# Kernel optimization log

Measured on AMD Instinct MI355X. Metric: run time of the kernel, lower is better.

Reference implementation:

```python
import jax, jax.numpy as jnp
import numpy as np

K = 20
EPS = 1e-5
NEG_SLOPE = 0.2


def knn(x, k):
    # x: [B, C, N] -> idx [B, N, k] of nearest neighbors (negative sq-dist topk)
    inner = -2.0 * jnp.einsum('bcn,bcm->bnm', x, x)
    xx = jnp.sum(x * x, axis=1)  # [B, N]
    d = -xx[:, :, None] - inner - xx[:, None, :]
    return jax.lax.top_k(d, k)[1]


def get_graph_feature(x, k):
    # x: [B, C, N] -> [B, 2C, N, k]
    idx = knn(x, k)
    xt = jnp.transpose(x, (0, 2, 1))            # [B, N, C]
    feat = jax.vmap(lambda a, i: a[i])(xt, idx)  # [B, N, k, C]
    center = xt[:, :, None, :]
    out = jnp.concatenate([feat - center, jnp.broadcast_to(center, feat.shape)], axis=-1)
    return jnp.transpose(out, (0, 3, 1, 2))


def conv_bn_lrelu(x, w, g, b):
    # 1x1 conv + BatchNorm2d (batch stats, training mode) + LeakyReLU(0.2)
    y = jnp.einsum('oc,bcnk->bonk', w, x)
    mu = jnp.mean(y, axis=(0, 2, 3), keepdims=True)
    var = jnp.mean((y - mu) ** 2, axis=(0, 2, 3), keepdims=True)
    y = (y - mu) * jax.lax.rsqrt(var + EPS)
    y = y * g[None, :, None, None] + b[None, :, None, None]
    return jnp.where(y >= 0, y, NEG_SLOPE * y)


def lrelu(y):
    return jnp.where(y >= 0, y, NEG_SLOPE * y)


def setup_inputs() -> dict:
    key = jax.random.key(0)
    ks = jax.random.split(key, 24)
    B, N = 8, 4096
    d = {}
    d['x'] = jax.random.normal(ks[0], (B, 3, N), dtype=jnp.float32)
    def wconv(k_, o, c):
        return jax.random.normal(k_, (o, c), dtype=jnp.float32) * (1.0 / np.sqrt(c))
    d['w1'] = wconv(ks[1], 32, 6)
    d['g1'] = 1.0 + 0.1 * jax.random.normal(ks[2], (32,), dtype=jnp.float32)
    d['b1'] = 0.1 * jax.random.normal(ks[3], (32,), dtype=jnp.float32)
    d['w2'] = wconv(ks[4], 64, 70)
    d['g2'] = 1.0 + 0.1 * jax.random.normal(ks[5], (64,), dtype=jnp.float32)
    d['b2'] = 0.1 * jax.random.normal(ks[6], (64,), dtype=jnp.float32)
    d['wd1'] = wconv(ks[7], 64, 64)
    d['gd1'] = 1.0 + 0.1 * jax.random.normal(ks[8], (64,), dtype=jnp.float32)
    d['bd1'] = 0.1 * jax.random.normal(ks[9], (64,), dtype=jnp.float32)
    d['wd2'] = wconv(ks[10], 64, 128)
    d['gd2'] = 1.0 + 0.1 * jax.random.normal(ks[11], (64,), dtype=jnp.float32)
    d['bd2'] = 0.1 * jax.random.normal(ks[12], (64,), dtype=jnp.float32)
    d['W2d'] = jax.random.normal(ks[13], (128, 128), dtype=jnp.float32) * (1.0 / np.sqrt(128))
    d['b2d'] = 0.1 * jax.random.normal(ks[14], (128,), dtype=jnp.float32)
    d['W3d'] = jax.random.normal(ks[15], (64, 128), dtype=jnp.float32) * (1.0 / np.sqrt(128))
    d['b3d'] = 0.1 * jax.random.normal(ks[16], (64,), dtype=jnp.float32)
    d['W4d'] = jax.random.normal(ks[17], (11, 64), dtype=jnp.float32) * (1.0 / np.sqrt(64))
    d['b4d'] = 0.1 * jax.random.normal(ks[18], (11,), dtype=jnp.float32)
    return d


def reference(x, w1, g1, b1, w2, g2, b2, wd1, gd1, bd1, wd2, gd2, bd2,
              W2d, b2d, W3d, b3d, W4d, b4d):
    x1_gf = get_graph_feature(x, K)                    # [B, 6, N, k]
    x1_max = jnp.max(conv_bn_lrelu(x1_gf, w1, g1, b1), axis=-1)  # [B, 32, N]
    x2_gf = jnp.concatenate([x1_gf, get_graph_feature(x1_max, K)], axis=1)  # [B, 70, N, k]
    x2_max = jnp.max(conv_bn_lrelu(x2_gf, w2, g2, b2), axis=-1)  # [B, 64, N]
    xd1 = jnp.max(conv_bn_lrelu(get_graph_feature(x1_max, K), wd1, gd1, bd1), axis=-1)  # [B, 64, N]
    xd2 = jnp.max(conv_bn_lrelu(get_graph_feature(x2_max, K), wd2, gd2, bd2), axis=-1)  # [B, 64, N]
    h = jnp.concatenate([xd1, xd2], axis=1)            # [B, 128, N]
    h = h.reshape(1, -1, 128)                          # faithful row-major view
    h = jnp.mean(h, axis=1)                            # [1, 128]
    h = lrelu(h @ W2d.T + b2d)
    h = lrelu(h @ W3d.T + b3d)
    return lrelu(h @ W4d.T + b4d)                      # [1, 11]
```

## Files before the change

kernel.cpp:

```cpp
#include <hip/hip_runtime.h>

#define BB 8
#define NN 4096
#define KK 20
constexpr float EPSV = 1e-5f;
constexpr float SLOPE = 0.2f;

typedef __bf16 bfrag __attribute__((ext_vector_type(8)));
typedef float floatx4 __attribute__((ext_vector_type(4)));
typedef unsigned short us4 __attribute__((ext_vector_type(4)));
typedef unsigned short us8 __attribute__((ext_vector_type(8)));

__device__ __forceinline__ float lrelu(float v) { return v >= 0.f ? v : SLOPE * v; }

__device__ __forceinline__ unsigned short bf16rn(float f) {
    unsigned int u = __float_as_uint(f);
    return (unsigned short)((u + 0x7FFFu + ((u >> 16) & 1u)) >> 16);
}
__device__ __forceinline__ float bf16up(unsigned short h) {
    return __uint_as_float(((unsigned int)h) << 16);
}

__device__ __forceinline__ void gl_lds16(const unsigned short* g, unsigned short* l) {
    __builtin_amdgcn_global_load_lds((const __attribute__((address_space(1))) void*)g,
                                     (__attribute__((address_space(3))) void*)l, 16, 0, 0);
}

__global__ void zero_kernel(float* p, int n) {
    int i = blockIdx.x * 256 + threadIdx.x;
    if (i < n) p[i] = 0.f;
}

template<int C>
__global__ void halfnorm_kernel(const float* __restrict__ src, float* __restrict__ hng) {
    int n = blockIdx.x * 256 + threadIdx.x;
    int b = blockIdx.y;
    float s = 0.f;
    #pragma unroll
    for (int c = 0; c < C; c++) { float v = src[(b * C + c) * NN + n]; s += v * v; }
    hng[b * NN + n] = 0.5f * s;
}

template<int C>
__global__ void pack_kernel(const float* __restrict__ src, const float* __restrict__ hng,
                            unsigned short* __restrict__ pk) {
    constexpr int SK = 2 * C + 8;
    const int b = blockIdx.y;
    const int m0 = blockIdx.x * 64;
    const int tid = threadIdx.x;
    for (int i = tid; i < 64 * (C / 4); i += 256) {
        int m = i & 63;
        int c4 = (i >> 6) * 4;
        us4 hv, lv;
        #pragma unroll
        for (int j = 0; j < 4; j++) {
            float v = src[(b * C + c4 + j) * NN + m0 + m];
            unsigned short h = bf16rn(v);
            hv[j] = h;
            lv[j] = bf16rn(v - bf16up(h));
        }
        *(us4*)(&pk[(size_t)(b * NN + m0 + m) * SK + c4]) = hv;
        *(us4*)(&pk[(size_t)(b * NN + m0 + m) * SK + C + c4]) = lv;
    }
    if (tid < 64) {
        unsigned int ub = __float_as_uint(hng[b * NN + m0 + tid]);
        us8 z;
        #pragma unroll
        for (int j = 0; j < 8; j++) z[j] = 0;
        z[0] = (unsigned short)(ub & 0xFFFFu);
        z[1] = (unsigned short)(ub >> 16);
        *(us8*)(&pk[(size_t)(b * NN + m0 + tid) * SK + 2 * C]) = z;
    }
}

__global__ void pack3_kernel(const float* __restrict__ src, const float* __restrict__ hng,
                             unsigned short* __restrict__ pk) {
    const int b = blockIdx.y;
    const int m = blockIdx.x * 256 + threadIdx.x;
    us8 w0, w1;
    #pragma unroll
    for (int j = 0; j < 8; j++) { w0[j] = 0; w1[j] = 0; }
    unsigned short row[12];
    #pragma unroll
    for (int c = 0; c < 3; c++) {
        float v = src[(b * 3 + c) * NN + m];
        unsigned short h = bf16rn(v);
        unsigned short l = bf16rn(v - bf16up(h));
        row[c] = h; row[3 + c] = l; row[6 + c] = l; row[9 + c] = h;
    }
    #pragma unroll
    for (int j = 0; j < 8; j++) w0[j] = row[j];
    #pragma unroll
    for (int j = 0; j < 4; j++) w1[j] = row[8 + j];
    unsigned short* dst = pk + (size_t)(b * NN + m) * 40;
    us8 z;
    #pragma unroll
    for (int j = 0; j < 8; j++) z[j] = 0;
    unsigned int ub = __float_as_uint(hng[b * NN + m]);
    us8 zh = z;
    zh[0] = (unsigned short)(ub & 0xFFFFu);
    zh[1] = (unsigned short)(ub >> 16);
    *(us8*)(dst) = w0;
    *(us8*)(dst + 8) = w1;
    *(us8*)(dst + 16) = z;
    *(us8*)(dst + 24) = z;
    *(us8*)(dst + 32) = zh;
}

template<int C>
__global__ __launch_bounds__(256) void knn_kernel(const float* __restrict__ src,
                                                  const unsigned short* __restrict__ pk,
                                                  int* __restrict__ idx) {
    constexpr int SK = (C == 3) ? 40 : (2 * C + 8);
    constexpr int HNOFF = (C == 3) ? 32 : 2 * C;
    constexpr int UNITS = 8 * SK;
    constexpr int PF = (UNITS + 255) / 256;
    constexpr int KKN = (C == 3) ? 1 : (C / 32);
    __shared__ __attribute__((aligned(16))) unsigned short cpack[2 * 64 * SK];
    __shared__ float pv[64 * 65];
    __shared__ unsigned short pidx[64 * 66];
    __shared__ float tau[64];
    __shared__ int cnt[64];
    __shared__ unsigned short qls[(C == 3) ? 64 * 40 : 2];

    const int bid = blockIdx.x;
    const int b = bid & 7;
    const int q0 = (bid >> 3) * 64;
    const int tid = threadIdx.x;
    const int lane = tid & 63;
    const int wv = tid >> 6;
    const int wr = (wv >> 1) * 32;
    const int wc = (wv & 1) * 32;
    const int fl = lane & 15;
    const int fq = lane >> 4;

    float tv[20]; int ti[20];
    #pragma unroll
    for (int k = 0; k < 20; k++) { tv[k] = -3.4e38f; ti[k] = 0; }

    bfrag qah[KKN][2], qal[KKN][2];
    if (C == 3) {
        for (int i = tid; i < 64 * 20; i += 256) {
            int r = i / 20, k = 12 + i % 20;
            qls[r * 40 + k] = 0;
        }
        if (tid < 64) {
            #pragma unroll
            for (int c = 0; c < 3; c++) {
                float v = src[(b * 3 + c) * NN + q0 + tid];
                unsigned short h = bf16rn(v);
                unsigned short l = bf16rn(v - bf16up(h));
                qls[tid * 40 + c] = h;  qls[tid * 40 + 3 + c] = l;
                qls[tid * 40 + 6 + c] = h;  qls[tid * 40 + 9 + c] = l;
            }
        }
    } else {
        #pragma unroll
        for (int r2 = 0; r2 < 2; r2++) {
            const unsigned short* qr = pk + (size_t)(b * NN + q0 + wr + r2 * 16 + fl) * SK + fq * 8;
            #pragma unroll
            for (int kk = 0; kk < KKN; kk++) {
                qah[kk][r2] = *(const bfrag*)(qr + kk * 32);
                qal[kk][r2] = *(const bfrag*)(qr + C + kk * 32);
            }
        }
    }

    {
        const unsigned short* p0 = pk + (size_t)(b * NN) * SK;
        #pragma unroll
        for (int r = 0; r < PF; r++) {
            int u0 = r * 256 + wv * 64;
            if (u0 < UNITS)
                gl_lds16(p0 + (size_t)(u0 + lane) * 8, cpack + (size_t)u0 * 8);
        }
    }
    if (tid < 64) { tau[tid] = -3.4e38f; cnt[tid] = 0; }
    __syncthreads();

    bfrag qa3[2];
    if (C == 3) {
        #pragma unroll
        for (int r2 = 0; r2 < 2; r2++)
            qa3[r2] = *(const bfrag*)(&qls[(wr + r2 * 16 + fl) * 40 + fq * 8]);
    }

    int buf = 0;
    for (int ch = 0; ch < 64; ch++) {
        unsigned short* cur = cpack + buf * (64 * SK);
        if (ch + 1 < 64) {
            unsigned short* nxt = cpack + (buf ^ 1) * (64 * SK);
            const unsigned short* pn = pk + (size_t)(b * NN + (ch + 1) * 64) * SK;
            #pragma unroll
            for (int r = 0; r < PF; r++) {
                int u0 = r * 256 + wv * 64;
                if (u0 < UNITS)
                    gl_lds16(pn + (size_t)(u0 + lane) * 8, nxt + (size_t)u0 * 8);
            }
        }

        floatx4 acc[2][2];
        #pragma unroll
        for (int r2 = 0; r2 < 2; r2++)
            #pragma unroll
            for (int c2 = 0; c2 < 2; c2++)
                acc[r2][c2] = (floatx4)(0.f);

        if (C == 3) {
            #pragma unroll
            for (int c2 = 0; c2 < 2; c2++) {
                bfrag bm = *(const bfrag*)(&cur[(wc + c2 * 16 + fl) * SK + fq * 8]);
                #pragma unroll
                for (int r2 = 0; r2 < 2; r2++)
                    acc[r2][c2] = __builtin_amdgcn_mfma_f32_16x16x32_bf16(qa3[r2], bm, acc[r2][c2], 0, 0, 0);
            }
        } else {
            #pragma unroll
            for (int kk = 0; kk < KKN; kk++) {
                const int kb = kk * 32 + fq * 8;
                bfrag bh[2], bl[2];
                #pragma unroll
                for (int c2 = 0; c2 < 2; c2++) {
                    bh[c2] = *(const bfrag*)(&cur[(wc + c2 * 16 + fl) * SK + kb]);
                    bl[c2] = *(const bfrag*)(&cur[(wc + c2 * 16 + fl) * SK + C + kb]);
                }
                #pragma unroll
                for (int r2 = 0; r2 < 2; r2++)
                    #pragma unroll
                    for (int c2 = 0; c2 < 2; c2++) {
                        acc[r2][c2] = __builtin_amdgcn_mfma_f32_16x16x32_bf16(qah[kk][r2], bh[c2], acc[r2][c2], 0, 0, 0);
                        acc[r2][c2] = __builtin_amdgcn_mfma_f32_16x16x32_bf16(qah[kk][r2], bl[c2], acc[r2][c2], 0, 0, 0);
                        acc[r2][c2] = __builtin_amdgcn_mfma_f32_16x16x32_bf16(qal[kk][r2], bh[c2], acc[r2][c2], 0, 0, 0);
                        acc[r2][c2] = __builtin_amdgcn_mfma_f32_16x16x32_bf16(qal[kk][r2], bl[c2], acc[r2][c2], 0, 0, 0);
                    }
            }
        }

        {
            const int m0 = ch * 64;
            float hvv[2];
            #pragma unroll
            for (int c2 = 0; c2 < 2; c2++)
                hvv[c2] = *(const float*)(&cur[(wc + c2 * 16 + fl) * SK + HNOFF]);
            #pragma unroll
            for (int r2 = 0; r2 < 2; r2++) {
                const int qb = wr + r2 * 16 + fq * 4;
                float4 t4 = *(const float4*)(&tau[qb]);
                float ta[4] = { t4.x, t4.y, t4.z, t4.w };
                #pragma unroll
                for (int c2 = 0; c2 < 2; c2++) {
                    const float hv = hvv[c2];
                    const int mm = m0 + wc + c2 * 16 + fl;
                    #pragma unroll
                    for (int reg = 0; reg < 4; reg++) {
                        float s = acc[r2][c2][reg] - hv;
                        if (s > ta[reg]) {
                            int q = qb + reg;
                            int p = atomicAdd(&cnt[q], 1);
                            pv[q * 65 + p] = s;
                            pidx[q * 66 + p] = (unsigned short)mm;
                        }
                    }
                }
            }
        }
        __syncthreads();

        if (tid < 64) {
            int n = cnt[tid];
            for (int t = 0; t < n; t++) {
                float v = pv[tid * 65 + t];
                if (v > tv[0]) {
                    tv[0] = v; ti[0] = (int)pidx[tid * 66 + t];
                    #pragma unroll
                    for (int j = 0; j < 19; j++) {
                        if (tv[j] > tv[j + 1]) {
                            float a = tv[j]; tv[j] = tv[j + 1]; tv[j + 1] = a;
                            int bi = ti[j]; ti[j] = ti[j + 1]; ti[j + 1] = bi;
                        }
                    }
                }
            }
            cnt[tid] = 0;
            tau[tid] = tv[0];
        }
        __syncthreads();
        buf ^= 1;
    }

    if (tid < 64) {
        #pragma unroll
        for (int k = 0; k < 20; k++)
            idx[(b * NN + q0 + tid) * KK + k] = ti[k];
    }
}

template<int COUT>
__global__ void precompute_kernel(const float* __restrict__ src, int C,
                                  const float* __restrict__ w, int CIN, int wd_off, int wc_off,
                                  float* __restrict__ G, float* __restrict__ H,
                                  int initG, int initH) {
    constexpr int MY = 256 / COUT;
    extern __shared__ float lds[];
    float* wd = lds;
    float* wc = lds + C * COUT;
    const int b = blockIdx.y;
    const int tid = threadIdx.y * COUT + threadIdx.x;
    for (int i = tid; i < C * COUT; i += 256) {
        int c = i / COUT, o = i % COUT;
        float a  = w[o * CIN + wd_off + c];
        float cc = w[o * CIN + wc_off + c];
        wd[i] = a;
        wc[i] = cc - a;
    }
    __syncthreads();
    const int o = threadIdx.x;
    for (int it = 0; it < COUT / 4; it++) {
        int m = blockIdx.x * 64 + it * MY + threadIdx.y;
        float g = 0.f, h = 0.f;
        for (int c = 0; c < C; c++) {
            float s = src[(b * C + c) * NN + m];
            g += wd[c * COUT + o] * s;
            h += wc[c * COUT + o] * s;
        }
        int gi = (b * NN + m) * COUT + o;
        if (initG) G[gi] = g; else G[gi] += g;
        if (initH) H[gi] = h; else H[gi] += h;
    }
}

template<int COUT, int GROUPS>
__global__ void conv_stats_kernel(const float* __restrict__ G1, const int* __restrict__ idx1,
                                  const float* __restrict__ G2, const int* __restrict__ idx2,
                                  const float* __restrict__ H, float* __restrict__ stats,
                                  float* __restrict__ MaxY, float* __restrict__ MinY) {
    constexpr int NY = 256 / COUT;
    const int b = blockIdx.y;
    const int o = threadIdx.x;
    const int n = blockIdx.x * NY + threadIdx.y;
    const int base = b * NN + n;
    const float h = H[base * COUT + o];
    float s1 = 0.f, s2 = 0.f;
    float gx = -3.4e38f, gn = 3.4e38f;
    #pragma unroll
    for (int k = 0; k < KK; k++) {
        int i1 = idx1[base * KK + k];
        float g = G1[(b * NN + i1) * COUT + o];
        if (GROUPS == 2) {
            int i2 = idx2[base * KK + k];
            g += G2[(b * NN + i2) * COUT + o];
        }
        float y = g + h;
        s1 += y;
        s2 += y * y;
        gx = fmaxf(gx, g);
        gn = fminf(gn, g);
    }
    MaxY[base * COUT + o] = gx + h;
    MinY[base * COUT + o] = gn + h;

    __shared__ float ls[2 * COUT];
    if (threadIdx.y == 0) { ls[o] = 0.f; ls[COUT + o] = 0.f; }
    __syncthreads();
    atomicAdd(&ls[o], s1);
    atomicAdd(&ls[COUT + o], s2);
    __syncthreads();
    if (threadIdx.y == 0) {
        atomicAdd(&stats[o], ls[o]);
        atomicAdd(&stats[64 + o], ls[COUT + o]);
    }
}

__global__ void finalize_kernel(const float* __restrict__ g, const float* __restrict__ bb,
                                float* __restrict__ stats, int cout, float invP) {
    int o = threadIdx.x;
    if (o >= cout) return;
    float mu  = stats[o] * invP;
    float var = stats[64 + o] * invP - mu * mu;
    float sc  = g[o] * rsqrtf(var + EPSV);
    stats[128 + o] = sc;
    stats[192 + o] = bb[o] - mu * sc;
}

__global__ void apply_kernel(const float* __restrict__ MaxY, const float* __restrict__ MinY,
                             const float* __restrict__ stats, float* __restrict__ out, int cout) {
    int e = blockIdx.x * 256 + threadIdx.x;
    int total = BB * cout * NN;
    if (e >= total) return;
    int n = e & (NN - 1);
    int o = (e >> 12) % cout;
    int b = e / (NN * cout);
    float sc = stats[128 + o], sh = stats[192 + o];
    int si = (b * NN + n) * cout + o;
    float v = (sc >= 0.f) ? MaxY[si] : MinY[si];
    out[e] = lrelu(sc * v + sh);
}

__global__ void mean_kernel(const float* __restrict__ xd1, const float* __restrict__ xd2,
                            float* __restrict__ hsum) {
    __shared__ float bins[128];
    const int tid = threadIdx.x;
    if (tid < 128) bins[tid] = 0.f;
    __syncthreads();
    const int half = BB * 64 * NN;
    const int stride = gridDim.x * 256;
    for (int e = blockIdx.x * 256 + tid; e < half; e += stride)
        atomicAdd(&bins[e & 127], xd1[e]);
    for (int e = blockIdx.x * 256 + tid; e < half; e += stride)
        atomicAdd(&bins[e & 127], xd2[e]);
    __syncthreads();
    if (tid < 128) atomicAdd(&hsum[tid], bins[tid]);
}

__global__ void head_kernel(const float* __restrict__ hsum,
                            const float* __restrict__ W2d, const float* __restrict__ b2d,
                            const float* __restrict__ W3d, const float* __restrict__ b3d,
                            const float* __restrict__ W4d, const float* __restrict__ b4d,
                            float* __restrict__ out) {
    __shared__ float h[128], t1[128], t2[64];
    const int t = threadIdx.x;
    h[t] = hsum[t] * (1.f / 32768.f);
    __syncthreads();
    float a = b2d[t];
    for (int j = 0; j < 128; j++) a += W2d[t * 128 + j] * h[j];
    t1[t] = lrelu(a);
    __syncthreads();
    if (t < 64) {
        float a2 = b3d[t];
        for (int j = 0; j < 128; j++) a2 += W3d[t * 128 + j] * t1[j];
        t2[t] = lrelu(a2);
    }
    __syncthreads();
    if (t < 11) {
        float a3 = b4d[t];
        for (int j = 0; j < 64; j++) a3 += W4d[t * 64 + j] * t2[j];
        out[t] = lrelu(a3);
    }
}

extern "C" void kernel_launch(void* const* d_in, const int* in_sizes, int n_in,
                              void* d_out, int out_size, void* d_ws, size_t ws_size,
                              hipStream_t stream) {
    const float* x   = (const float*)d_in[0];
    const float* w1  = (const float*)d_in[1];
    const float* g1  = (const float*)d_in[2];
    const float* b1  = (const float*)d_in[3];
    const float* w2  = (const float*)d_in[4];
    const float* g2  = (const float*)d_in[5];
    const float* b2  = (const float*)d_in[6];
    const float* wd1 = (const float*)d_in[7];
    const float* gd1 = (const float*)d_in[8];
    const float* bd1 = (const float*)d_in[9];
    const float* wd2 = (const float*)d_in[10];
    const float* gd2 = (const float*)d_in[11];
    const float* bd2 = (const float*)d_in[12];
    const float* W2d = (const float*)d_in[13];
    const float* b2d = (const float*)d_in[14];
    const float* W3d = (const float*)d_in[15];
    const float* b3d = (const float*)d_in[16];
    const float* W4d = (const float*)d_in[17];
    const float* b4d = (const float*)d_in[18];
    float* out = (float*)d_out;

    char* ws = (char*)d_ws;
    size_t off = 0;
    auto alloc = [&](size_t bytes) { char* p = ws + off; off += (bytes + 255) & ~size_t(255); return p; };
    int*   idx1  = (int*)  alloc(BB * NN * KK * 4);
    int*   idx2  = (int*)  alloc(BB * NN * KK * 4);
    int*   idx3  = (int*)  alloc(BB * NN * KK * 4);
    float* x1m   = (float*)alloc(BB * 32 * NN * 4);
    float* x2m   = (float*)alloc(BB * 64 * NN * 4);
    float* xd1   = (float*)alloc(BB * 64 * NN * 4);
    float* xd2   = (float*)alloc(BB * 64 * NN * 4);
    float* G1    = (float*)alloc((size_t)BB * NN * 64 * 4);
    float* G2    = (float*)alloc((size_t)BB * NN * 64 * 4);
    float* H     = (float*)alloc((size_t)BB * NN * 64 * 4);
    float* MaxY  = (float*)alloc((size_t)BB * NN * 64 * 4);
    float* MinY  = (float*)alloc((size_t)BB * NN * 64 * 4);
    float* stats = (float*)alloc(256 * 4);
    float* hsum  = (float*)alloc(128 * 4);
    float* hng   = (float*)alloc(BB * NN * 4);

    unsigned short* pkbuf = (unsigned short*)MaxY;

    const float invP = 1.f / (float)(BB * NN * KK);
    const dim3 knn_grid(NN / 64 * BB);
    const dim3 hn_grid(NN / 256, BB);

    zero_kernel<<<1, 256, 0, stream>>>(hsum, 128);

    halfnorm_kernel<3><<<hn_grid, 256, 0, stream>>>(x, hng);
    pack3_kernel<<<dim3(NN / 256, BB), 256, 0, stream>>>(x, hng, pkbuf);
    knn_kernel<3><<<knn_grid, 256, 0, stream>>>(x, pkbuf, idx1);

    zero_kernel<<<1, 256, 0, stream>>>(stats, 128);
    precompute_kernel<32><<<dim3(NN / 64, BB), dim3(32, 8), 2 * 3 * 32 * 4, stream>>>(
        x, 3, w1, 6, 0, 3, G1, H, 1, 1);
    conv_stats_kernel<32, 1><<<dim3(NN / 8, BB), dim3(32, 8), 0, stream>>>(
        G1, idx1, nullptr, nullptr, H, stats, MaxY, MinY);
    finalize_kernel<<<1, 64, 0, stream>>>(g1, b1, stats, 32, invP);
    apply_kernel<<<(BB * 32 * NN + 255) / 256, 256, 0, stream>>>(MaxY, MinY, stats, x1m, 32);

    halfnorm_kernel<32><<<hn_grid, 256, 0, stream>>>(x1m, hng);
    pack_kernel<32><<<dim3(NN / 64, BB), 256, 0, stream>>>(x1m, hng, pkbuf);
    knn_kernel<32><<<knn_grid, 256, 0, stream>>>(x1m, pkbuf, idx2);

    zero_kernel<<<1, 256, 0, stream>>>(stats, 128);
    precompute_kernel<64><<<dim3(NN / 64, BB), dim3(64, 4), 2 * 3 * 64 * 4, stream>>>(
        x, 3, w2, 70, 0, 3, G1, H, 1, 1);
    precompute_kernel<64><<<dim3(NN / 64, BB), dim3(64, 4), 2 * 32 * 64 * 4, stream>>>(
        x1m, 32, w2, 70, 6, 38, G2, H, 1, 0);
    conv_stats_kernel<64, 2><<<dim3(NN / 4, BB), dim3(64, 4), 0, stream>>>(
        G1, idx1, G2, idx2, H, stats, MaxY, MinY);
    finalize_kernel<<<1, 64, 0, stream>>>(g2, b2, stats, 64, invP);
    apply_kernel<<<(BB * 64 * NN + 255) / 256, 256, 0, stream>>>(MaxY, MinY, stats, x2m, 64);

    zero_kernel<<<1, 256, 0, stream>>>(stats, 128);
    precompute_kernel<64><<<dim3(NN / 64, BB), dim3(64, 4), 2 * 32 * 64 * 4, stream>>>(
        x1m, 32, wd1, 64, 0, 32, G1, H, 1, 1);
    conv_stats_kernel<64, 1><<<dim3(NN / 4, BB), dim3(64, 4), 0, stream>>>(
        G1, idx2, nullptr, nullptr, H, stats, MaxY, MinY);
    finalize_kernel<<<1, 64, 0, stream>>>(gd1, bd1, stats, 64, invP);
    apply_kernel<<<(BB * 64 * NN + 255) / 256, 256, 0, stream>>>(MaxY, MinY, stats, xd1, 64);

    halfnorm_kernel<64><<<hn_grid, 256, 0, stream>>>(x2m, hng);
    pack_kernel<64><<<dim3(NN / 64, BB), 256, 0, stream>>>(x2m, hng, pkbuf);
    knn_kernel<64><<<knn_grid, 256, 0, stream>>>(x2m, pkbuf, idx3);

    zero_kernel<<<1, 256, 0, stream>>>(stats, 128);
    precompute_kernel<64><<<dim3(NN / 64, BB), dim3(64, 4), 2 * 64 * 64 * 4, stream>>>(
        x2m, 64, wd2, 128, 0, 64, G1, H, 1, 1);
    conv_stats_kernel<64, 1><<<dim3(NN / 4, BB), dim3(64, 4), 0, stream>>>(
        G1, idx3, nullptr, nullptr, H, stats, MaxY, MinY);
    finalize_kernel<<<1, 64, 0, stream>>>(gd2, bd2, stats, 64, invP);
    apply_kernel<<<(BB * 64 * NN + 255) / 256, 256, 0, stream>>>(MaxY, MinY, stats, xd2, 64);

    mean_kernel<<<1024, 256, 0, stream>>>(xd1, xd2, hsum);
    head_kernel<<<1, 128, 0, stream>>>(hsum, W2d, b2d, W3d, b3d, W4d, b4d, out);
}
```

Before: 1.706 ms.

## Double KNN block query tile and overlap top-k merge with next MFMA chunk

The KNN kernel now handles 128 queries per block with 512 threads, so each candidate chunk loaded into LDS is reused across twice as many queries. The per-chunk top-k insertion pass, which ran between two barriers, now runs at the start of the next iteration and reads candidates from a 128-entry ring buffer using a running lo/hi count. This removes one barrier per chunk and lets the serial merge by 128 threads overlap with MFMA work in the other waves. The trade-offs are that tau is one chunk staler, which admits more candidates, the ring can overflow if more than 128 candidates build up per query before a merge, and the grid has half as many blocks.

```diff
diff --git a/kernel.cpp b/kernel.cpp
--- a/kernel.cpp
+++ b/kernel.cpp
@@ -108,24 +108,25 @@
 }
 
 template<int C>
-__global__ __launch_bounds__(256) void knn_kernel(const float* __restrict__ src,
+__global__ __launch_bounds__(512) void knn_kernel(const float* __restrict__ src,
                                                   const unsigned short* __restrict__ pk,
                                                   int* __restrict__ idx) {
     constexpr int SK = (C == 3) ? 40 : (2 * C + 8);
     constexpr int HNOFF = (C == 3) ? 32 : 2 * C;
     constexpr int UNITS = 8 * SK;
-    constexpr int PF = (UNITS + 255) / 256;
+    constexpr int CHUNK = 64 * SK;
+    constexpr int RU = (UNITS + 511) / 512;
     constexpr int KKN = (C == 3) ? 1 : (C / 32);
-    __shared__ __attribute__((aligned(16))) unsigned short cpack[2 * 64 * SK];
-    __shared__ float pv[64 * 65];
-    __shared__ unsigned short pidx[64 * 66];
-    __shared__ float tau[64];
-    __shared__ int cnt[64];
-    __shared__ unsigned short qls[(C == 3) ? 64 * 40 : 2];
+    constexpr int PVS = 130, PIS = 129;
+    __shared__ __attribute__((aligned(16))) unsigned short cpack[2 * CHUNK];
+    __shared__ __attribute__((aligned(16))) float pv[128 * PVS];
+    __shared__ unsigned short pidx[128 * PIS];
+    __shared__ float tau[128];
+    __shared__ int cnt[128];
 
     const int bid = blockIdx.x;
     const int b = bid & 7;
-    const int q0 = (bid >> 3) * 64;
+    const int q0 = (bid >> 3) * 128;
     const int tid = threadIdx.x;
     const int lane = tid & 63;
     const int wv = tid >> 6;
@@ -140,11 +141,10 @@
 
     bfrag qah[KKN][2], qal[KKN][2];
     if (C == 3) {
-        for (int i = tid; i < 64 * 20; i += 256) {
-            int r = i / 20, k = 12 + i % 20;
-            qls[r * 40 + k] = 0;
-        }
-        if (tid < 64) {
+        unsigned short* qls = (unsigned short*)pv;
+        if (tid < 128) {
+            #pragma unroll
+            for (int k2 = 12; k2 < 32; k2++) qls[tid * 40 + k2] = 0;
             #pragma unroll
             for (int c = 0; c < 3; c++) {
                 float v = src[(b * 3 + c) * NN + q0 + tid];
@@ -169,34 +169,56 @@
     {
         const unsigned short* p0 = pk + (size_t)(b * NN) * SK;
         #pragma unroll
-        for (int r = 0; r < PF; r++) {
-            int u0 = r * 256 + wv * 64;
+        for (int r = 0; r < RU; r++) {
+            int u0 = r * 512 + wv * 64;
             if (u0 < UNITS)
                 gl_lds16(p0 + (size_t)(u0 + lane) * 8, cpack + (size_t)u0 * 8);
         }
     }
-    if (tid < 64) { tau[tid] = -3.4e38f; cnt[tid] = 0; }
+    if (tid < 128) { tau[tid] = -3.4e38f; cnt[tid] = 0; }
     __syncthreads();
 
     bfrag qa3[2];
     if (C == 3) {
+        const unsigned short* qls = (const unsigned short*)pv;
         #pragma unroll
         for (int r2 = 0; r2 < 2; r2++)
             qa3[r2] = *(const bfrag*)(&qls[(wr + r2 * 16 + fl) * 40 + fq * 8]);
-    }
-
-    int buf = 0;
+        __syncthreads();
+    }
+
+    int lo = 0;
     for (int ch = 0; ch < 64; ch++) {
-        unsigned short* cur = cpack + buf * (64 * SK);
+        const unsigned short* cur = cpack + (ch & 1) * CHUNK;
         if (ch + 1 < 64) {
-            unsigned short* nxt = cpack + (buf ^ 1) * (64 * SK);
+            unsigned short* nxt = cpack + ((ch + 1) & 1) * CHUNK;
             const unsigned short* pn = pk + (size_t)(b * NN + (ch + 1) * 64) * SK;
             #pragma unroll
-            for (int r = 0; r < PF; r++) {
-                int u0 = r * 256 + wv * 64;
+            for (int r = 0; r < RU; r++) {
+                int u0 = r * 512 + wv * 64;
                 if (u0 < UNITS)
                     gl_lds16(pn + (size_t)(u0 + lane) * 8, nxt + (size_t)u0 * 8);
             }
+        }
+
+        if (tid < 128) {
+            int hi = cnt[tid];
+            for (int t = lo; t < hi; t++) {
+                int s = t & 127;
+                float v = pv[tid * PVS + s];
+                if (v > tv[0]) {
+                    tv[0] = v; ti[0] = (int)pidx[tid * PIS + s];
+                    #pragma unroll
+                    for (int j = 0; j < 19; j++) {
+                        if (tv[j] > tv[j + 1]) {
+                            float a = tv[j]; tv[j] = tv[j + 1]; tv[j + 1] = a;
+                            int bi = ti[j]; ti[j] = ti[j + 1]; ti[j + 1] = bi;
+                        }
+                    }
+                }
+            }
+            lo = hi;
+            tau[tid] = tv[0];
         }
 
         floatx4 acc[2][2];
@@ -257,38 +279,33 @@
                         if (s > ta[reg]) {
                             int q = qb + reg;
                             int p = atomicAdd(&cnt[q], 1);
-                            pv[q * 65 + p] = s;
-                            pidx[q * 66 + p] = (unsigned short)mm;
+                            int sl = p & 127;
+                            pv[q * PVS + sl] = s;
+                            pidx[q * PIS + sl] = (unsigned short)mm;
                         }
                     }
                 }
             }
         }
         __syncthreads();
-
-        if (tid < 64) {
-            int n = cnt[tid];
-            for (int t = 0; t < n; t++) {
-                float v = pv[tid * 65 + t];
-                if (v > tv[0]) {
-                    tv[0] = v; ti[0] = (int)pidx[tid * 66 + t];
-                    #pragma unroll
-                    for (int j = 0; j < 19; j++) {
-                        if (tv[j] > tv[j + 1]) {
-                            float a = tv[j]; tv[j] = tv[j + 1]; tv[j + 1] = a;
-                            int bi = ti[j]; ti[j] = ti[j + 1]; ti[j + 1] = bi;
-                        }
+    }
+
+    if (tid < 128) {
+        int hi = cnt[tid];
+        for (int t = lo; t < hi; t++) {
+            int s = t & 127;
+            float v = pv[tid * PVS + s];
+            if (v > tv[0]) {
+                tv[0] = v; ti[0] = (int)pidx[tid * PIS + s];
+                #pragma unroll
+                for (int j = 0; j < 19; j++) {
+                    if (tv[j] > tv[j + 1]) {
+                        float a = tv[j]; tv[j] = tv[j + 1]; tv[j + 1] = a;
+                        int bi = ti[j]; ti[j] = ti[j + 1]; ti[j + 1] = bi;
                     }
                 }
             }
-            cnt[tid] = 0;
-            tau[tid] = tv[0];
-        }
-        __syncthreads();
-        buf ^= 1;
-    }
-
-    if (tid < 64) {
+        }
         #pragma unroll
         for (int k = 0; k < 20; k++)
             idx[(b * NN + q0 + tid) * KK + k] = ti[k];
@@ -484,14 +501,14 @@
     unsigned short* pkbuf = (unsigned short*)MaxY;
 
     const float invP = 1.f / (float)(BB * NN * KK);
-    const dim3 knn_grid(NN / 64 * BB);
+    const dim3 knn_grid(NN / 128 * BB);
     const dim3 hn_grid(NN / 256, BB);
 
     zero_kernel<<<1, 256, 0, stream>>>(hsum, 128);
 
     halfnorm_kernel<3><<<hn_grid, 256, 0, stream>>>(x, hng);
     pack3_kernel<<<dim3(NN / 256, BB), 256, 0, stream>>>(x, hng, pkbuf);
-    knn_kernel<3><<<knn_grid, 256, 0, stream>>>(x, pkbuf, idx1);
+    knn_kernel<3><<<knn_grid, 512, 0, stream>>>(x, pkbuf, idx1);
 
     zero_kernel<<<1, 256, 0, stream>>>(stats, 128);
     precompute_kernel<32><<<dim3(NN / 64, BB), dim3(32, 8), 2 * 3 * 32 * 4, stream>>>(
@@ -503,7 +520,7 @@
 
     halfnorm_kernel<32><<<hn_grid, 256, 0, stream>>>(x1m, hng);
     pack_kernel<32><<<dim3(NN / 64, BB), 256, 0, stream>>>(x1m, hng, pkbuf);
-    knn_kernel<32><<<knn_grid, 256, 0, stream>>>(x1m, pkbuf, idx2);
+    knn_kernel<32><<<knn_grid, 512, 0, stream>>>(x1m, pkbuf, idx2);
 
     zero_kernel<<<1, 256, 0, stream>>>(stats, 128);
     precompute_kernel<64><<<dim3(NN / 64, BB), dim3(64, 4), 2 * 3 * 64 * 4, stream>>>(
@@ -525,7 +542,7 @@
 
     halfnorm_kernel<64><<<hn_grid, 256, 0, stream>>>(x2m, hng);
     pack_kernel<64><<<dim3(NN / 64, BB), 256, 0, stream>>>(x2m, hng, pkbuf);
-    knn_kernel<64><<<knn_grid, 256, 0, stream>>>(x2m, pkbuf, idx3);
+    knn_kernel<64><<<knn_grid, 512, 0, stream>>>(x2m, pkbuf, idx3);
 
     zero_kernel<<<1, 256, 0, stream>>>(stats, 128);
     precompute_kernel<64><<<dim3(NN / 64, BB), dim3(64, 4), 2 * 64 * 64 * 4, stream>>>(
```

Result: slower. 1.769 ms (+3.7%).

## Deepen kNN candidate prefetch to two chunks with explicit vmcnt waits

Applied to the files above, without the earlier changes.

The kNN kernel now preloads the first two candidate chunks and, inside the loop, issues the global-to-LDS load for chunk ch+2 right after the scoring barrier, so it overlaps the serial top-k merge. The full __syncthreads barriers are replaced by s_barrier plus targeted s_waitcnt vmcnt/lgkmcnt, so each wave waits only for its own older loads. The vmcnt values depend on how many loads each wave issues per chunk (wave 0 issues one more), which makes the code fragile if any other global memory op lands in the loop.

```diff
diff --git a/kernel.cpp b/kernel.cpp
--- a/kernel.cpp
+++ b/kernel.cpp
@@ -24,6 +24,18 @@
 __device__ __forceinline__ void gl_lds16(const unsigned short* g, unsigned short* l) {
     __builtin_amdgcn_global_load_lds((const __attribute__((address_space(1))) void*)g,
                                      (__attribute__((address_space(3))) void*)l, 16, 0, 0);
+}
+
+template<int N> __device__ __forceinline__ void wait_vm() {
+    if constexpr (N == 0)      asm volatile("s_waitcnt vmcnt(0)");
+    else if constexpr (N == 1) asm volatile("s_waitcnt vmcnt(1)");
+    else if constexpr (N == 2) asm volatile("s_waitcnt vmcnt(2)");
+    else if constexpr (N == 3) asm volatile("s_waitcnt vmcnt(3)");
+    else if constexpr (N == 4) asm volatile("s_waitcnt vmcnt(4)");
+    else                       asm volatile("s_waitcnt vmcnt(5)");
+}
+__device__ __forceinline__ void wait_lgkm0() {
+    asm volatile("s_waitcnt lgkmcnt(0)" ::: "memory");
 }
 
 __global__ void zero_kernel(float* p, int n) {
@@ -114,9 +126,10 @@
     constexpr int SK = (C == 3) ? 40 : (2 * C + 8);
     constexpr int HNOFF = (C == 3) ? 32 : 2 * C;
     constexpr int UNITS = 8 * SK;
-    constexpr int PF = (UNITS + 255) / 256;
+    constexpr int CHUNK = 64 * SK;
+    constexpr int RU = (UNITS + 255) / 256;
     constexpr int KKN = (C == 3) ? 1 : (C / 32);
-    __shared__ __attribute__((aligned(16))) unsigned short cpack[2 * 64 * SK];
+    __shared__ __attribute__((aligned(16))) unsigned short cpack[2 * CHUNK];
     __shared__ float pv[64 * 65];
     __shared__ unsigned short pidx[64 * 66];
     __shared__ float tau[64];
@@ -169,14 +182,23 @@
     {
         const unsigned short* p0 = pk + (size_t)(b * NN) * SK;
         #pragma unroll
-        for (int r = 0; r < PF; r++) {
+        for (int r = 0; r < RU; r++) {
             int u0 = r * 256 + wv * 64;
             if (u0 < UNITS)
                 gl_lds16(p0 + (size_t)(u0 + lane) * 8, cpack + (size_t)u0 * 8);
         }
+        const unsigned short* p1 = pk + (size_t)(b * NN + 64) * SK;
+        #pragma unroll
+        for (int r = 0; r < RU; r++) {
+            int u0 = r * 256 + wv * 64;
+            if (u0 < UNITS)
+                gl_lds16(p1 + (size_t)(u0 + lane) * 8, cpack + (size_t)(CHUNK * 1) + (size_t)u0 * 8 - CHUNK + CHUNK);
+        }
     }
     if (tid < 64) { tau[tid] = -3.4e38f; cnt[tid] = 0; }
-    __syncthreads();
+    wait_lgkm0();
+    if (wv == 0) wait_vm<RU>(); else wait_vm<RU - 1>();
+    __builtin_amdgcn_s_barrier();
 
     bfrag qa3[2];
     if (C == 3) {
@@ -185,19 +207,8 @@
             qa3[r2] = *(const bfrag*)(&qls[(wr + r2 * 16 + fl) * 40 + fq * 8]);
     }
 
-    int buf = 0;
     for (int ch = 0; ch < 64; ch++) {
-        unsigned short* cur = cpack + buf * (64 * SK);
-        if (ch + 1 < 64) {
-            unsigned short* nxt = cpack + (buf ^ 1) * (64 * SK);
-            const unsigned short* pn = pk + (size_t)(b * NN + (ch + 1) * 64) * SK;
-            #pragma unroll
-            for (int r = 0; r < PF; r++) {
-                int u0 = r * 256 + wv * 64;
-                if (u0 < UNITS)
-                    gl_lds16(pn + (size_t)(u0 + lane) * 8, nxt + (size_t)u0 * 8);
-            }
-        }
+        const unsigned short* cur = cpack + (ch & 1) * CHUNK;
 
         floatx4 acc[2][2];
         #pragma unroll
@@ -264,8 +275,19 @@
                 }
             }
         }
-        __syncthreads();
-
+        wait_lgkm0();
+        __builtin_amdgcn_s_barrier();
+
+        if (ch + 2 < 64) {
+            unsigned short* dst = cpack + (ch & 1) * CHUNK;
+            const unsigned short* pn = pk + (size_t)(b * NN + (ch + 2) * 64) * SK;
+            #pragma unroll
+            for (int r = 0; r < RU; r++) {
+                int u0 = r * 256 + wv * 64;
+                if (u0 < UNITS)
+                    gl_lds16(pn + (size_t)(u0 + lane) * 8, dst + (size_t)u0 * 8);
+            }
+        }
         if (tid < 64) {
             int n = cnt[tid];
             for (int t = 0; t < n; t++) {
@@ -284,8 +306,12 @@
             cnt[tid] = 0;
             tau[tid] = tv[0];
         }
-        __syncthreads();
-        buf ^= 1;
+        wait_lgkm0();
+        if (ch + 1 < 64) {
+            if (ch + 2 < 64) { if (wv == 0) wait_vm<RU>(); else wait_vm<RU - 1>(); }
+            else             wait_vm<0>();
+        }
+        __builtin_amdgcn_s_barrier();
     }
 
     if (tid < 64) {
```

Measured after the change: 1.783 ms. 1.05x slower.

## Fuse half-norm into pack kernels, batch-interleave grids, merge stats zeroing

Applied to the files above, without the earlier changes.

Removes the separate halfnorm kernels by computing the half squared norm inside the pack kernels. Flattens 2D grids into 1D grids with the batch index in the low bits, so consecutive blocks span different batches, which may change cache locality. Uses four separate stats buffers cleared by a single zero launch instead of one per stage. The aim is fewer launches and less intermediate traffic; in exchange, a few threads in pack_kernel now recompute the norm with a serial loop over channels.

```diff
diff --git a/kernel.cpp b/kernel.cpp
--- a/kernel.cpp
+++ b/kernel.cpp
@@ -32,21 +32,11 @@
 }
 
 template<int C>
-__global__ void halfnorm_kernel(const float* __restrict__ src, float* __restrict__ hng) {
-    int n = blockIdx.x * 256 + threadIdx.x;
-    int b = blockIdx.y;
-    float s = 0.f;
-    #pragma unroll
-    for (int c = 0; c < C; c++) { float v = src[(b * C + c) * NN + n]; s += v * v; }
-    hng[b * NN + n] = 0.5f * s;
-}
-
-template<int C>
-__global__ void pack_kernel(const float* __restrict__ src, const float* __restrict__ hng,
-                            unsigned short* __restrict__ pk) {
+__global__ void pack_kernel(const float* __restrict__ src, unsigned short* __restrict__ pk) {
     constexpr int SK = 2 * C + 8;
-    const int b = blockIdx.y;
-    const int m0 = blockIdx.x * 64;
+    const int id = blockIdx.x;
+    const int b = id & 7;
+    const int m0 = (id >> 3) * 64;
     const int tid = threadIdx.x;
     for (int i = tid; i < 64 * (C / 4); i += 256) {
         int m = i & 63;
@@ -63,7 +53,12 @@
         *(us4*)(&pk[(size_t)(b * NN + m0 + m) * SK + C + c4]) = lv;
     }
     if (tid < 64) {
-        unsigned int ub = __float_as_uint(hng[b * NN + m0 + tid]);
+        float s = 0.f;
+        for (int c = 0; c < C; c++) {
+            float v = src[(b * C + c) * NN + m0 + tid];
+            s += v * v;
+        }
+        unsigned int ub = __float_as_uint(0.5f * s);
         us8 z;
         #pragma unroll
         for (int j = 0; j < 8; j++) z[j] = 0;
@@ -73,17 +68,19 @@
     }
 }
 
-__global__ void pack3_kernel(const float* __restrict__ src, const float* __restrict__ hng,
-                             unsigned short* __restrict__ pk) {
-    const int b = blockIdx.y;
-    const int m = blockIdx.x * 256 + threadIdx.x;
+__global__ void pack3_kernel(const float* __restrict__ src, unsigned short* __restrict__ pk) {
+    const int id = blockIdx.x;
+    const int b = id & 7;
+    const int m = (id >> 3) * 256 + threadIdx.x;
     us8 w0, w1;
     #pragma unroll
     for (int j = 0; j < 8; j++) { w0[j] = 0; w1[j] = 0; }
     unsigned short row[12];
+    float s = 0.f;
     #pragma unroll
     for (int c = 0; c < 3; c++) {
         float v = src[(b * 3 + c) * NN + m];
+        s += v * v;
         unsigned short h = bf16rn(v);
         unsigned short l = bf16rn(v - bf16up(h));
         row[c] = h; row[3 + c] = l; row[6 + c] = l; row[9 + c] = h;
@@ -96,7 +93,7 @@
     us8 z;
     #pragma unroll
     for (int j = 0; j < 8; j++) z[j] = 0;
-    unsigned int ub = __float_as_uint(hng[b * NN + m]);
+    unsigned int ub = __float_as_uint(0.5f * s);
     us8 zh = z;
     zh[0] = (unsigned short)(ub & 0xFFFFu);
     zh[1] = (unsigned short)(ub >> 16);
@@ -304,7 +301,9 @@
     extern __shared__ float lds[];
     float* wd = lds;
     float* wc = lds + C * COUT;
-    const int b = blockIdx.y;
+    const int id = blockIdx.x;
+    const int b = id & 7;
+    const int m_base = (id >> 3) * 64;
     const int tid = threadIdx.y * COUT + threadIdx.x;
     for (int i = tid; i < C * COUT; i += 256) {
         int c = i / COUT, o = i % COUT;
@@ -316,7 +315,7 @@
     __syncthreads();
     const int o = threadIdx.x;
     for (int it = 0; it < COUT / 4; it++) {
-        int m = blockIdx.x * 64 + it * MY + threadIdx.y;
+        int m = m_base + it * MY + threadIdx.y;
         float g = 0.f, h = 0.f;
         for (int c = 0; c < C; c++) {
             float s = src[(b * C + c) * NN + m];
@@ -335,9 +334,10 @@
                                   const float* __restrict__ H, float* __restrict__ stats,
                                   float* __restrict__ MaxY, float* __restrict__ MinY) {
     constexpr int NY = 256 / COUT;
-    const int b = blockIdx.y;
+    const int id = blockIdx.x;
+    const int b = id & 7;
     const int o = threadIdx.x;
-    const int n = blockIdx.x * NY + threadIdx.y;
+    const int n = (id >> 3) * NY + threadIdx.y;
     const int base = b * NN + n;
     const float h = H[base * COUT + o];
     float s1 = 0.f, s2 = 0.f;
@@ -384,16 +384,16 @@
 
 __global__ void apply_kernel(const float* __restrict__ MaxY, const float* __restrict__ MinY,
                              const float* __restrict__ stats, float* __restrict__ out, int cout) {
-    int e = blockIdx.x * 256 + threadIdx.x;
-    int total = BB * cout * NN;
-    if (e >= total) return;
+    const int id = blockIdx.x;
+    const int b = id & 7;
+    int e = (id >> 3) * 256 + threadIdx.x;
+    if (e >= cout * NN) return;
     int n = e & (NN - 1);
-    int o = (e >> 12) % cout;
-    int b = e / (NN * cout);
+    int o = e >> 12;
     float sc = stats[128 + o], sh = stats[192 + o];
     int si = (b * NN + n) * cout + o;
     float v = (sc >= 0.f) ? MaxY[si] : MinY[si];
-    out[e] = lrelu(sc * v + sh);
+    out[(b * cout + o) * NN + n] = lrelu(sc * v + sh);
 }
 
 __global__ void mean_kernel(const float* __restrict__ xd1, const float* __restrict__ xd2,
@@ -477,63 +477,60 @@
     float* H     = (float*)alloc((size_t)BB * NN * 64 * 4);
     float* MaxY  = (float*)alloc((size_t)BB * NN * 64 * 4);
     float* MinY  = (float*)alloc((size_t)BB * NN * 64 * 4);
-    float* stats = (float*)alloc(256 * 4);
+    float* stats = (float*)alloc(4 * 256 * 4);
     float* hsum  = (float*)alloc(128 * 4);
-    float* hng   = (float*)alloc(BB * NN * 4);
+
+    float* st0 = stats;
+    float* st1 = stats + 256;
+    float* st2 = stats + 512;
+    float* st3 = stats + 768;
 
     unsigned short* pkbuf = (unsigned short*)MaxY;
 
     const float invP = 1.f / (float)(BB * NN * KK);
     const dim3 knn_grid(NN / 64 * BB);
-    const dim3 hn_grid(NN / 256, BB);
-
-    zero_kernel<<<1, 256, 0, stream>>>(hsum, 128);
-
-    halfnorm_kernel<3><<<hn_grid, 256, 0, stream>>>(x, hng);
-    pack3_kernel<<<dim3(NN / 256, BB), 256, 0, stream>>>(x, hng, pkbuf);
+    const dim3 pre_grid(NN / 64 * BB);
+
+    zero_kernel<<<5, 256, 0, stream>>>(stats, 1024 + 128);
+
+    pack3_kernel<<<NN / 256 * BB, 256, 0, stream>>>(x, pkbuf);
     knn_kernel<3><<<knn_grid, 256, 0, stream>>>(x, pkbuf, idx1);
 
-    zero_kernel<<<1, 256, 0, stream>>>(stats, 128);
-    precompute_kernel<32><<<dim3(NN / 64, BB), dim3(32, 8), 2 * 3 * 32 * 4, stream>>>(
+    precompute_kernel<32><<<pre_grid, dim3(32, 8), 2 * 3 * 32 * 4, stream>>>(
         x, 3, w1, 6, 0, 3, G1, H, 1, 1);
-    conv_stats_kernel<32, 1><<<dim3(NN / 8, BB), dim3(32, 8), 0, stream>>>(
-        G1, idx1, nullptr, nullptr, H, stats, MaxY, MinY);
-    finalize_kernel<<<1, 64, 0, stream>>>(g1, b1, stats, 32, invP);
-    apply_kernel<<<(BB * 32 * NN + 255) / 256, 256, 0, stream>>>(MaxY, MinY, stats, x1m, 32);
-
-    halfnorm_kernel<32><<<hn_grid, 256, 0, stream>>>(x1m, hng);
-    pack_kernel<32><<<dim3(NN / 64, BB), 256, 0, stream>>>(x1m, hng, pkbuf);
+    conv_stats_kernel<32, 1><<<NN / 8 * BB, dim3(32, 8), 0, stream>>>(
+        G1, idx1, nullptr, nullptr, H, st0, MaxY, MinY);
+    finalize_kernel<<<1, 64, 0, stream>>>(g1, b1, st0, 32, invP);
+    apply_kernel<<<32 * NN / 256 * BB, 256, 0, stream>>>(MaxY, MinY, st0, x1m, 32);
+
+    pack_kernel<32><<<pre_grid, 256, 0, stream>>>(x1m, pkbuf);
     knn_kernel<32><<<knn_grid, 256, 0, stream>>>(x1m, pkbuf, idx2);
 
-    zero_kernel<<<1, 256, 0, stream>>>(stats, 128);
-    precompute_kernel<64><<<dim3(NN / 64, BB), dim3(64, 4), 2 * 3 * 64 * 4, stream>>>(
+    precompute_kernel<64><<<pre_grid, dim3(64, 4), 2 * 3 * 64 * 4, stream>>>(
         x, 3, w2, 70, 0, 3, G1, H, 1, 1);
-    precompute_kernel<64><<<dim3(NN / 64, BB), dim3(64, 4), 2 * 32 * 64 * 4, stream>>>(
+    precompute_kernel<64><<<pre_grid, dim3(64, 4), 2 * 32 * 64 * 4, stream>>>(
         x1m, 32, w2, 70, 6, 38, G2, H, 1, 0);
-    conv_stats_kernel<64, 2><<<dim3(NN / 4, BB), dim3(64, 4), 0, stream>>>(
-        G1, idx1, G2, idx2, H, stats, MaxY, MinY);
-    finalize_kernel<<<1, 64, 0, stream>>>(g2, b2, stats, 64, invP);
-    apply_kernel<<<(BB * 64 * NN + 255) / 256, 256, 0, stream>>>(MaxY, MinY, stats, x2m, 64);
-
-    zero_kernel<<<1, 256, 0, stream>>>(stats, 128);
-    precompute_kernel<64><<<dim3(NN / 64, BB), dim3(64, 4), 2 * 32 * 64 * 4, stream>>>(
+    conv_stats_kernel<64, 2><<<NN / 4 * BB, dim3(64, 4), 0, stream>>>(
+        G1, idx1, G2, idx2, H, st1, MaxY, MinY);
+    finalize_kernel<<<1, 64, 0, stream>>>(g2, b2, st1, 64, invP);
+    apply_kernel<<<64 * NN / 256 * BB, 256, 0, stream>>>(MaxY, MinY, st1, x2m, 64);
+
+    precompute_kernel<64><<<pre_grid, dim3(64, 4), 2 * 32 * 64 * 4, stream>>>(
         x1m, 32, wd1, 64, 0, 32, G1, H, 1, 1);
-    conv_stats_kernel<64, 1><<<dim3(NN / 4, BB), dim3(64, 4), 0, stream>>>(
-        G1, idx2, nullptr, nullptr, H, stats, MaxY, MinY);
-    finalize_kernel<<<1, 64, 0, stream>>>(gd1, bd1, stats, 64, invP);
-    apply_kernel<<<(BB * 64 * NN + 255) / 256, 256, 0, stream>>>(MaxY, MinY, stats, xd1, 64);
-
-    halfnorm_kernel<64><<<hn_grid, 256, 0, stream>>>(x2m, hng);
-    pack_kernel<64><<<dim3(NN / 64, BB), 256, 0, stream>>>(x2m, hng, pkbuf);
+    conv_stats_kernel<64, 1><<<NN / 4 * BB, dim3(64, 4), 0, stream>>>(
+        G1, idx2, nullptr, nullptr, H, st2, MaxY, MinY);
+    finalize_kernel<<<1, 64, 0, stream>>>(gd1, bd1, st2, 64, invP);
+    apply_kernel<<<64 * NN / 256 * BB, 256, 0, stream>>>(MaxY, MinY, st2, xd1, 64);
+
+    pack_kernel<64><<<pre_grid, 256, 0, stream>>>(x2m, pkbuf);
     knn_kernel<64><<<knn_grid, 256, 0, stream>>>(x2m, pkbuf, idx3);
 
-    zero_kernel<<<1, 256, 0, stream>>>(stats, 128);
-    precompute_kernel<64><<<dim3(NN / 64, BB), dim3(64, 4), 2 * 64 * 64 * 4, stream>>>(
+    precompute_kernel<64><<<pre_grid, dim3(64, 4), 2 * 64 * 64 * 4, stream>>>(
         x2m, 64, wd2, 128, 0, 64, G1, H, 1, 1);
-    conv_stats_kernel<64, 1><<<dim3(NN / 4, BB), dim3(64, 4), 0, stream>>>(
-        G1, idx3, nullptr, nullptr, H, stats, MaxY, MinY);
-    finalize_kernel<<<1, 64, 0, stream>>>(gd2, bd2, stats, 64, invP);
-    apply_kernel<<<(BB * 64 * NN + 255) / 256, 256, 0, stream>>>(MaxY, MinY, stats, xd2, 64);
+    conv_stats_kernel<64, 1><<<NN / 4 * BB, dim3(64, 4), 0, stream>>>(
+        G1, idx3, nullptr, nullptr, H, st3, MaxY, MinY);
+    finalize_kernel<<<1, 64, 0, stream>>>(gd2, bd2, st3, 64, invP);
+    apply_kernel<<<64 * NN / 256 * BB, 256, 0, stream>>>(MaxY, MinY, st3, xd2, 64);
 
     mean_kernel<<<1024, 256, 0, stream>>>(xd1, xd2, hsum);
     head_kernel<<<1, 128, 0, stream>>>(hsum, W2d, b2d, W3d, b3d, W4d, b4d, out);
```

New measurement: 1.670 ms. -2.2%, faster.
